# Kernel tuning notes

Hardware: AMD Instinct MI355X
Metric: run time of the kernel (lower is better)

The kernel has to match this reference:

```python
import jax, jax.numpy as jnp
import numpy as np

D_MODEL = 128
NHEAD = 8
HEAD_DIM = D_MODEL // NHEAD  # 16
NUM_LAYERS = 7
NUM_LABELS = 2
N_NODES = 10000
N_EDGES = 160000
NEG_SLOPE = 0.2  # GATv2Conv default negative_slope


def setup_inputs() -> dict:
    key = jax.random.key(0)
    ks = jax.random.split(key, 10)
    s = 1.0 / np.sqrt(D_MODEL)
    inp = {}
    inp["x"] = jax.random.normal(ks[0], (N_NODES, D_MODEL), dtype=jnp.float32)
    inp["edge_index"] = jax.random.randint(ks[1], (2, N_EDGES), 0, N_NODES, dtype=jnp.int64)
    inp["nchunks"] = 8  # uniform extra chunk size -> chunk = NUM_LABELS + 8 = 10
    # per-layer GATv2 params, stacked on a leading layer axis
    inp["Wl"] = jax.random.normal(ks[2], (NUM_LAYERS, D_MODEL, NHEAD * HEAD_DIM), dtype=jnp.float32) * s
    inp["bl"] = jnp.zeros((NUM_LAYERS, NHEAD * HEAD_DIM), dtype=jnp.float32)
    inp["Wr"] = jax.random.normal(ks[3], (NUM_LAYERS, D_MODEL, NHEAD * HEAD_DIM), dtype=jnp.float32) * s
    inp["br"] = jnp.zeros((NUM_LAYERS, NHEAD * HEAD_DIM), dtype=jnp.float32)
    inp["att"] = jax.random.normal(ks[4], (NUM_LAYERS, NHEAD, HEAD_DIM), dtype=jnp.float32) * s
    inp["bias"] = jnp.zeros((NUM_LAYERS, NHEAD * HEAD_DIM), dtype=jnp.float32)
    # split head: Linear(d_model, 1)
    inp["w_head"] = jax.random.normal(ks[5], (D_MODEL, 1), dtype=jnp.float32) * s
    inp["b_head"] = jnp.zeros((1,), dtype=jnp.float32)
    return inp


def _gatv2_layer(x, src, dst, Wl, bl, Wr, br, att, bias):
    # GATv2: e_ij = a^T LeakyReLU(W_l x_j + W_r x_i); alpha = segment-softmax over dst; out_i = sum alpha * W_l x_j
    N = x.shape[0]
    xl = (x @ Wl + bl).reshape(N, NHEAD, HEAD_DIM)
    xr = (x @ Wr + br).reshape(N, NHEAD, HEAD_DIM)
    z = jax.nn.leaky_relu(xl[src] + xr[dst], NEG_SLOPE)          # [E, H, D]
    e = jnp.einsum('ehd,hd->eh', z, att)                          # [E, H]
    emax = jax.ops.segment_max(e, dst, num_segments=N)            # [N, H]
    ex = jnp.exp(e - emax[dst])
    denom = jax.ops.segment_sum(ex, dst, num_segments=N)          # [N, H]
    alpha = ex / (denom[dst] + 1e-16)                             # [E, H]
    out = jax.ops.segment_sum(alpha[..., None] * xl[src], dst, num_segments=N)  # [N, H, D]
    return out.reshape(N, NHEAD * HEAD_DIM) + bias


def reference(x, edge_index, nchunks, Wl, bl, Wr, br, att, bias, w_head, b_head):
    N = x.shape[0]
    loop = jnp.arange(N, dtype=edge_index.dtype)  # GATv2Conv add_self_loops=True
    src = jnp.concatenate([edge_index[0], loop])
    dst = jnp.concatenate([edge_index[1], loop])
    for i in range(NUM_LAYERS):
        x = _gatv2_layer(x, src, dst, Wl[i], bl[i], Wr[i], br[i], att[i], bias[i])
    # uniform split of size (NUM_LABELS + nchunks); keep first NUM_LABELS rows of each chunk
    chunk = NUM_LABELS + int(nchunks)
    xs = x.reshape(-1, chunk, D_MODEL)[:, :NUM_LABELS]            # [n_chunks, num_labels, d]
    out = (xs @ w_head + b_head)[..., 0]                          # [n_chunks, num_labels]
    return out
```

## Files before the change

### kernel.cpp

```cpp
#include <hip/hip_runtime.h>
#include <math.h>

typedef __attribute__((ext_vector_type(8))) short bf16x8;
typedef __attribute__((ext_vector_type(4))) float f32x4;

#define WFRAG (16 * 4 * 64 * 8)


__device__ inline int detect_is64(const int* __restrict__ ei) {
    int is64 = 1;
#pragma unroll
    for (int k = 1; k < 16; k += 2) is64 &= (ei[k] == 0);
    return is64;
}

__device__ inline void split1(float f, short& hi, short& lo) {
    unsigned u = __float_as_uint(f);
    hi = (short)(u >> 16);
    float fl = f - __uint_as_float(u & 0xffff0000u);
    lo = (short)(__float_as_uint(fl) >> 16);
}

__device__ inline void cvt8(const float4& a, const float4& b, bf16x8& hi, bf16x8& lo) {
    float f[8] = {a.x, a.y, a.z, a.w, b.x, b.y, b.z, b.w};
#pragma unroll
    for (int j = 0; j < 8; j++) {
        unsigned u = __float_as_uint(f[j]);
        hi[j] = (short)(u >> 16);
        float fl = f[j] - __uint_as_float(u & 0xffff0000u);
        lo[j] = (short)(__float_as_uint(fl) >> 16);
    }
}


__global__ __launch_bounds__(256) void prologue(const float* __restrict__ Wl,
                                                const float* __restrict__ Wr,
                                                short* __restrict__ Whi,
                                                short* __restrict__ Wlo,
                                                const float4* __restrict__ x4,
                                                short* __restrict__ cvH,
                                                short* __restrict__ cvL,
                                                const int* __restrict__ ei,
                                                int* __restrict__ deg,
                                                int N, int E) {
    __shared__ float Wt[128][17];
    int b = blockIdx.x, t = threadIdx.x;
    if (b < 112) {
        int l = b >> 4;
        int tile = b & 15;
        int c0 = tile * 16;
        const float* Wsrc = (c0 < 128) ? Wl + (size_t)l * 16384 : Wr + (size_t)l * 16384;
        int cbase = (c0 < 128) ? c0 : c0 - 128;
#pragma unroll
        for (int it = 0; it < 8; it++) {
            int idx = it * 256 + t;
            int k = idx >> 4, c = idx & 15;
            Wt[k][c] = Wsrc[(size_t)k * 128 + cbase + c];
        }
        __syncthreads();
        int kt = t >> 6, lane = t & 63, q = (lane >> 4), cl = lane & 15;
        bf16x8 hi, lo;
#pragma unroll
        for (int j = 0; j < 8; j++) {
            short h, lw;
            split1(Wt[kt * 32 + q * 8 + j][cl], h, lw);
            hi[j] = h; lo[j] = lw;
        }
        size_t off = ((((size_t)l * 16 + tile) * 4 + kt) * 64 + lane) * 8;
        *(bf16x8*)(Whi + off) = hi;
        *(bf16x8*)(Wlo + off) = lo;
        return;
    }
    int rb = b - 112;
    int RB = gridDim.x - 112;
    int n8 = N * 16;
    for (int id = rb * 256 + t; id < n8; id += RB * 256) {
        float4 a = x4[2 * id];
        float4 bb = x4[2 * id + 1];
        bf16x8 h, lw;
        cvt8(a, bb, h, lw);
        *(bf16x8*)(cvH + (size_t)id * 8) = h;
        *(bf16x8*)(cvL + (size_t)id * 8) = lw;
    }
    int is64 = detect_is64(ei);
    for (int e = rb * 256 + t; e < E; e += RB * 256) {
        long long pos = (long long)E + e;
        int d = ei[is64 ? 2 * pos : pos];
        if ((unsigned)d < (unsigned)N) atomicAdd(&deg[d], 1);
    }
}


__global__ __launch_bounds__(1024) void scan_kernel(const int* __restrict__ deg,
                                                    int* __restrict__ off,
                                                    int* __restrict__ cur, int N) {
    __shared__ int wsum[16];
    int t = threadIdx.x;
    int per = (N + 1023) >> 10;
    int b0 = t * per;
    int s = 0;
    for (int k = 0; k < per; k++) {
        int idx = b0 + k;
        if (idx < N) s += deg[idx];
    }
    int lane = t & 63, w = t >> 6;
    int v = s;
#pragma unroll
    for (int o = 1; o < 64; o <<= 1) {
        int u = __shfl_up(v, o, 64);
        if (lane >= o) v += u;
    }
    if (lane == 63) wsum[w] = v;
    __syncthreads();
    if (t == 0) {
        int r = 0;
#pragma unroll
        for (int j = 0; j < 16; j++) { int xx = wsum[j]; wsum[j] = r; r += xx; }
        off[N] = r;
    }
    __syncthreads();
    int run = v - s + wsum[w];
    for (int k = 0; k < per; k++) {
        int idx = b0 + k;
        if (idx < N) {
            off[idx] = run;
            cur[idx] = run;
            run += deg[idx];
        }
    }
}

__global__ void fill_kernel(const int* __restrict__ ei, int E, int N,
                            int* __restrict__ cur, int* __restrict__ esrc) {
    int e = blockIdx.x * blockDim.x + threadIdx.x;
    if (e >= E) return;
    int is64 = detect_is64(ei);
    long long spos = e, dpos = (long long)E + e;
    int s = ei[is64 ? 2 * spos : spos];
    int d = ei[is64 ? 2 * dpos : dpos];
    if ((unsigned)d >= (unsigned)N || (unsigned)s >= (unsigned)N) return;
    int p = atomicAdd(&cur[d], 1);
    esrc[p] = s;
}


__global__ __launch_bounds__(512, 1) void gemm_xlxr(const short* __restrict__ xhi,
                                                    const short* __restrict__ xlo,
                                                    const short* __restrict__ WhiL,
                                                    const short* __restrict__ WloL,
                                                    const float* __restrict__ blv,
                                                    const float* __restrict__ brv,
                                                    float* __restrict__ xl,
                                                    float* __restrict__ xr,
                                                    int N, int ntiles) {
    int t = threadIdx.x;
    int w = t >> 6, lane = t & 63, q = lane >> 4, cl = lane & 15;

    bf16x8 Bh[2][4], Bl[2][4];
    float biasv[2];
    float* op[2];
    int colc[2];
#pragma unroll
    for (int nt = 0; nt < 2; nt++) {
        int tile = w * 2 + nt;
        int col = tile * 16 + cl;
        if (col < 128) { biasv[nt] = blv[col]; op[nt] = xl; colc[nt] = col; }
        else           { biasv[nt] = brv[col - 128]; op[nt] = xr; colc[nt] = col - 128; }
#pragma unroll
        for (int kt = 0; kt < 4; kt++) {
            size_t o = (((size_t)tile * 4 + kt) * 64 + lane) * 8;
            Bh[nt][kt] = *(const bf16x8*)(WhiL + o);
            Bl[nt][kt] = *(const bf16x8*)(WloL + o);
        }
    }

    for (int rt = blockIdx.x; rt < ntiles; rt += gridDim.x) {
        int row = rt * 16 + cl;
        if (row >= N) row = N - 1;
        const short* ph = xhi + (size_t)row * 128 + q * 8;
        const short* pl = xlo + (size_t)row * 128 + q * 8;
        bf16x8 AH[4], AL[4];
#pragma unroll
        for (int kt = 0; kt < 4; kt++) {
            AH[kt] = *(const bf16x8*)(ph + kt * 32);
            AL[kt] = *(const bf16x8*)(pl + kt * 32);
        }

        f32x4 acc0 = {0.f, 0.f, 0.f, 0.f}, acc1 = {0.f, 0.f, 0.f, 0.f};
#pragma unroll
        for (int kt = 0; kt < 4; kt++) {
            acc0 = __builtin_amdgcn_mfma_f32_16x16x32_bf16(AH[kt], Bh[0][kt], acc0, 0, 0, 0);
            acc1 = __builtin_amdgcn_mfma_f32_16x16x32_bf16(AH[kt], Bh[1][kt], acc1, 0, 0, 0);
            acc0 = __builtin_amdgcn_mfma_f32_16x16x32_bf16(AL[kt], Bh[0][kt], acc0, 0, 0, 0);
            acc1 = __builtin_amdgcn_mfma_f32_16x16x32_bf16(AL[kt], Bh[1][kt], acc1, 0, 0, 0);
            acc0 = __builtin_amdgcn_mfma_f32_16x16x32_bf16(AH[kt], Bl[0][kt], acc0, 0, 0, 0);
            acc1 = __builtin_amdgcn_mfma_f32_16x16x32_bf16(AH[kt], Bl[1][kt], acc1, 0, 0, 0);
        }

#pragma unroll
        for (int nt = 0; nt < 2; nt++) {
            f32x4 a = nt ? acc1 : acc0;
#pragma unroll
            for (int r = 0; r < 4; r++) {
                int orow = rt * 16 + q * 4 + r;
                if (orow < N) op[nt][(size_t)orow * 128 + colc[nt]] = a[r] + biasv[nt];
            }
        }
    }
}


__device__ inline void agg_node(int i, int sub, int cl,
                                const float4* __restrict__ xl4, const float4* __restrict__ xr4,
                                const int* __restrict__ off, const int* __restrict__ esrc,
                                float4 atA, float4 atB, float4 bA, float4 bB,
                                float4& oA, float4& oB) {
    float4 xrA = xr4[(size_t)i * 32 + 2 * cl];
    float4 xrB = xr4[(size_t)i * 32 + 2 * cl + 1];
    int start = off[i];
    int total = off[i + 1] - start + 1;
    int groups = (total + 3) >> 2;

    int k0 = sub;
    int s0 = (k0 < total) ? ((k0 == 0) ? i : esrc[start + k0 - 1]) : i;
    int k1 = 4 + sub;
    int s1 = (k1 < total) ? esrc[start + k1 - 1] : i;
    float4 v0A = xl4[(size_t)s0 * 32 + 2 * cl];
    float4 v0B = xl4[(size_t)s0 * 32 + 2 * cl + 1];
    int k2 = 8 + sub;
    int s2 = (k2 < total) ? esrc[start + k2 - 1] : i;
    float4 v1A = xl4[(size_t)s1 * 32 + 2 * cl];
    float4 v1B = xl4[(size_t)s1 * 32 + 2 * cl + 1];

    float s = 0.f;
    float4 aA = make_float4(0.f, 0.f, 0.f, 0.f);
    float4 aB = make_float4(0.f, 0.f, 0.f, 0.f);

    for (int g = 0; g < groups; g++) {
        int k3 = 4 * (g + 3) + sub;
        int s3 = (k3 < total) ? esrc[start + k3 - 1] : i;
        float4 v2A = xl4[(size_t)s2 * 32 + 2 * cl];
        float4 v2B = xl4[(size_t)s2 * 32 + 2 * cl + 1];

        int kc = 4 * g + sub;
        int valid = kc < total;
        float z0 = v0A.x + xrA.x, z1 = v0A.y + xrA.y, z2 = v0A.z + xrA.z, z3 = v0A.w + xrA.w;
        float z4 = v0B.x + xrB.x, z5 = v0B.y + xrB.y, z6 = v0B.z + xrB.z, z7 = v0B.w + xrB.w;
        z0 = (z0 > 0.f) ? z0 : 0.2f * z0;
        z1 = (z1 > 0.f) ? z1 : 0.2f * z1;
        z2 = (z2 > 0.f) ? z2 : 0.2f * z2;
        z3 = (z3 > 0.f) ? z3 : 0.2f * z3;
        z4 = (z4 > 0.f) ? z4 : 0.2f * z4;
        z5 = (z5 > 0.f) ? z5 : 0.2f * z5;
        z6 = (z6 > 0.f) ? z6 : 0.2f * z6;
        z7 = (z7 > 0.f) ? z7 : 0.2f * z7;
        float p = z0 * atA.x + z1 * atA.y + z2 * atA.z + z3 * atA.w
                + z4 * atB.x + z5 * atB.y + z6 * atB.z + z7 * atB.w;
        p += __shfl_xor(p, 1, 64);
        p = fminf(fmaxf(p, -80.f), 80.f);
        float wgt = valid ? __expf(p) : 0.f;
        s += wgt;
        aA.x += wgt * v0A.x; aA.y += wgt * v0A.y; aA.z += wgt * v0A.z; aA.w += wgt * v0A.w;
        aB.x += wgt * v0B.x; aB.y += wgt * v0B.y; aB.z += wgt * v0B.z; aB.w += wgt * v0B.w;

        v0A = v1A; v0B = v1B;
        v1A = v2A; v1B = v2B;
        s2 = s3;
    }

#pragma unroll
    for (int o = 16; o <= 32; o <<= 1) {
        s += __shfl_xor(s, o, 64);
        aA.x += __shfl_xor(aA.x, o, 64); aA.y += __shfl_xor(aA.y, o, 64);
        aA.z += __shfl_xor(aA.z, o, 64); aA.w += __shfl_xor(aA.w, o, 64);
        aB.x += __shfl_xor(aB.x, o, 64); aB.y += __shfl_xor(aB.y, o, 64);
        aB.z += __shfl_xor(aB.z, o, 64); aB.w += __shfl_xor(aB.w, o, 64);
    }
    float inv = 1.f / (s + 1e-16f);
    oA.x = aA.x * inv + bA.x; oA.y = aA.y * inv + bA.y;
    oA.z = aA.z * inv + bA.z; oA.w = aA.w * inv + bA.w;
    oB.x = aB.x * inv + bB.x; oB.y = aB.y * inv + bB.y;
    oB.z = aB.z * inv + bB.z; oB.w = aB.w * inv + bB.w;
}


__global__ __launch_bounds__(256) void agg_gemm(const float4* __restrict__ xl4,
                                                const float4* __restrict__ xr4,
                                                const int* __restrict__ off,
                                                const int* __restrict__ esrc,
                                                const float4* __restrict__ att4,
                                                const float4* __restrict__ bias4,
                                                const short* __restrict__ WhiL,
                                                const short* __restrict__ WloL,
                                                const float* __restrict__ blv,
                                                const float* __restrict__ brv,
                                                float* __restrict__ xlo_out,
                                                float* __restrict__ xro_out,
                                                int N) {
    __shared__ __align__(16) short hiL[16 * 136];
    __shared__ __align__(16) short loL[16 * 136];
    int t = threadIdx.x;
    int w = t >> 6, lane = t & 63, sub = lane >> 4, cl = lane & 15, q = lane >> 4;
    int base = blockIdx.x * 16;

    float4 atA = att4[2 * cl];
    float4 atB = att4[2 * cl + 1];
    float4 bA = bias4[2 * cl], bB = bias4[2 * cl + 1];

    for (int j = 0; j < 4; j++) {
        int i = base + w * 4 + j;
        if (i < N) {
            float4 oA, oB;
            agg_node(i, sub, cl, xl4, xr4, off, esrc, atA, atB, bA, bB, oA, oB);
            if (sub == 0) {
                bf16x8 h, lw;
                cvt8(oA, oB, h, lw);
                int r = w * 4 + j;
                *(bf16x8*)&hiL[r * 136 + cl * 8] = h;
                *(bf16x8*)&loL[r * 136 + cl * 8] = lw;
            }
        }
    }
    __syncthreads();

    bf16x8 Ah[4], Al[4];
#pragma unroll
    for (int kt = 0; kt < 4; kt++) {
        Ah[kt] = *(const bf16x8*)&hiL[cl * 136 + kt * 32 + q * 8];
        Al[kt] = *(const bf16x8*)&loL[cl * 136 + kt * 32 + q * 8];
    }

#pragma unroll
    for (int tt = 0; tt < 4; tt++) {
        int tile = w * 4 + tt;
        int col = tile * 16 + cl;
        f32x4 acc = {0.f, 0.f, 0.f, 0.f};
#pragma unroll
        for (int kt = 0; kt < 4; kt++) {
            size_t o = (((size_t)tile * 4 + kt) * 64 + lane) * 8;
            bf16x8 bh = *(const bf16x8*)(WhiL + o);
            bf16x8 bl2 = *(const bf16x8*)(WloL + o);
            acc = __builtin_amdgcn_mfma_f32_16x16x32_bf16(Ah[kt], bh, acc, 0, 0, 0);
            acc = __builtin_amdgcn_mfma_f32_16x16x32_bf16(Al[kt], bh, acc, 0, 0, 0);
            acc = __builtin_amdgcn_mfma_f32_16x16x32_bf16(Ah[kt], bl2, acc, 0, 0, 0);
        }
        float biasv;
        float* op;
        int cc;
        if (col < 128) { biasv = blv[col]; op = xlo_out; cc = col; }
        else           { biasv = brv[col - 128]; op = xro_out; cc = col - 128; }
#pragma unroll
        for (int r = 0; r < 4; r++) {
            int row = base + q * 4 + r;
            if (row < N) op[(size_t)row * 128 + cc] = acc[r] + biasv;
        }
    }
}


__global__ __launch_bounds__(256) void gat_agg(const float4* __restrict__ xl4,
                                               const float4* __restrict__ xr4,
                                               const int* __restrict__ off,
                                               const int* __restrict__ esrc,
                                               const float4* __restrict__ att4,
                                               const float4* __restrict__ bias4,
                                               float4* __restrict__ out4, int N) {
    int lane = threadIdx.x & 63;
    int sub = lane >> 4;
    int cl = lane & 15;
    int i = blockIdx.x * 4 + (threadIdx.x >> 6);
    if (i >= N) return;
    float4 atA = att4[2 * cl];
    float4 atB = att4[2 * cl + 1];
    float4 bA = bias4[2 * cl], bB = bias4[2 * cl + 1];
    float4 oA, oB;
    agg_node(i, sub, cl, xl4, xr4, off, esrc, atA, atB, bA, bB, oA, oB);
    if (sub == 0) {
        out4[(size_t)i * 32 + 2 * cl] = oA;
        out4[(size_t)i * 32 + 2 * cl + 1] = oB;
    }
}


__global__ __launch_bounds__(128) void head_kernel(const float* __restrict__ x,
                                                   const float* __restrict__ w,
                                                   const float* __restrict__ bh,
                                                   const int* __restrict__ nch,
                                                   float* __restrict__ out) {
    __shared__ float r[2];
    int b = blockIdx.x, t = threadIdx.x;
    int chunk = 2 + nch[0];
    int row = (b >> 1) * chunk + (b & 1);
    float p = x[(size_t)row * 128 + t] * w[t];
#pragma unroll
    for (int o = 32; o >= 1; o >>= 1) p += __shfl_xor(p, o, 64);
    if ((t & 63) == 0) r[t >> 6] = p;
    __syncthreads();
    if (t == 0) out[b] = r[0] + r[1] + bh[0];
}


extern "C" void kernel_launch(void* const* d_in, const int* in_sizes, int n_in,
                              void* d_out, int out_size, void* d_ws, size_t ws_size,
                              hipStream_t stream) {
    const float* x0 = (const float*)d_in[0];
    const int* ei = (const int*)d_in[1];
    const int* nchunks = (const int*)d_in[2];
    const float* Wl = (const float*)d_in[3];
    const float* bl = (const float*)d_in[4];
    const float* Wr = (const float*)d_in[5];
    const float* br = (const float*)d_in[6];
    const float* att = (const float*)d_in[7];
    const float* bias = (const float*)d_in[8];
    const float* wh = (const float*)d_in[9];
    const float* bh = (const float*)d_in[10];

    const int D = 128;
    int N = in_sizes[0] / D;
    int E = in_sizes[1] / 2;
    int ntiles = (N + 15) / 16;

    size_t fN = (size_t)N * D;
    float* xlA = (float*)d_ws;
    float* xrA = xlA + fN;
    float* xlB = xrA + fN;
    float* xrB = xlB + fN;
    float* xout = xrB + fN;
    short* cvH0 = (short*)(xout + fN);
    short* cvL0 = cvH0 + fN;
    short* Whi = cvL0 + fN;
    short* Wlo = Whi + 7 * (size_t)WFRAG;
    int* deg = (int*)(Wlo + 7 * (size_t)WFRAG);
    int* off = deg + N;
    int* cur = off + N + 1;
    int* esrc = cur + N;

    hipMemsetAsync(deg, 0, (size_t)N * sizeof(int), stream);
    prologue<<<112 + 640, 256, 0, stream>>>(Wl, Wr, Whi, Wlo, (const float4*)x0,
                                            cvH0, cvL0, ei, deg, N, E);
    scan_kernel<<<1, 1024, 0, stream>>>(deg, off, cur, N);
    fill_kernel<<<(E + 255) / 256, 256, 0, stream>>>(ei, E, N, cur, esrc);

    gemm_xlxr<<<256, 512, 0, stream>>>(cvH0, cvL0, Whi, Wlo, bl, br, xlA, xrA, N, ntiles);

    for (int l = 0; l < 6; l++) {
        const float* rxl = (l % 2 == 0) ? xlA : xlB;
        const float* rxr = (l % 2 == 0) ? xrA : xrB;
        float* wxl = (l % 2 == 0) ? xlB : xlA;
        float* wxr = (l % 2 == 0) ? xrB : xrA;
        agg_gemm<<<ntiles, 256, 0, stream>>>((const float4*)rxl, (const float4*)rxr, off, esrc,
                                             (const float4*)(att + (size_t)l * D),
                                             (const float4*)(bias + (size_t)l * D),
                                             Whi + (size_t)(l + 1) * WFRAG,
                                             Wlo + (size_t)(l + 1) * WFRAG,
                                             bl + (size_t)(l + 1) * D,
                                             br + (size_t)(l + 1) * D,
                                             wxl, wxr, N);
    }

    gat_agg<<<(N + 3) / 4, 256, 0, stream>>>((const float4*)xlA, (const float4*)xrA, off, esrc,
                                             (const float4*)(att + 6 * (size_t)D),
                                             (const float4*)(bias + 6 * (size_t)D),
                                             (float4*)xout, N);

    head_kernel<<<out_size, 128, 0, stream>>>(xout, wh, bh, nchunks, (float*)d_out);
}
```

Measured before the change: 272.8 us.

## Split fused agg+GEMM into head-sliced aggregation and separate GEMM kernels

Replaces the fused per-layer aggregation+MFMA GEMM kernel with two kernels. The first is a head-sliced aggregation: each block handles one head for 16 nodes, with 4 lanes per edge slot, and writes a bf16 hi/lo split. The second is a standalone GEMM with the weights held in registers. The scan is also merged with the first GEMM into one launch. This aims to raise parallelism and locality in the gather phase, at the cost of extra launches and an intermediate buffer round trip each layer.

```diff
diff --git a/kernel.cpp b/kernel.cpp
--- a/kernel.cpp
+++ b/kernel.cpp
@@ -2,6 +2,7 @@
 #include <math.h>
 
 typedef __attribute__((ext_vector_type(8))) short bf16x8;
+typedef __attribute__((ext_vector_type(4))) short short4v;
 typedef __attribute__((ext_vector_type(4))) float f32x4;
 
 #define WFRAG (16 * 4 * 64 * 8)
@@ -91,41 +92,173 @@
 }
 
 
-__global__ __launch_bounds__(1024) void scan_kernel(const int* __restrict__ deg,
-                                                    int* __restrict__ off,
-                                                    int* __restrict__ cur, int N) {
-    __shared__ int wsum[16];
+__global__ __launch_bounds__(512, 1) void scan_gemm0(const int* __restrict__ deg,
+                                                     int* __restrict__ offp,
+                                                     int* __restrict__ cur, int N,
+                                                     const short* __restrict__ xhi,
+                                                     const short* __restrict__ xlo,
+                                                     const short* __restrict__ WhiL,
+                                                     const short* __restrict__ WloL,
+                                                     const float* __restrict__ blv,
+                                                     const float* __restrict__ brv,
+                                                     float* __restrict__ xl,
+                                                     float* __restrict__ xr,
+                                                     int ntiles) {
+    __shared__ int wsum[8];
     int t = threadIdx.x;
-    int per = (N + 1023) >> 10;
-    int b0 = t * per;
-    int s = 0;
-    for (int k = 0; k < per; k++) {
-        int idx = b0 + k;
-        if (idx < N) s += deg[idx];
-    }
-    int lane = t & 63, w = t >> 6;
-    int v = s;
-#pragma unroll
-    for (int o = 1; o < 64; o <<= 1) {
-        int u = __shfl_up(v, o, 64);
-        if (lane >= o) v += u;
-    }
-    if (lane == 63) wsum[w] = v;
-    __syncthreads();
-    if (t == 0) {
-        int r = 0;
-#pragma unroll
-        for (int j = 0; j < 16; j++) { int xx = wsum[j]; wsum[j] = r; r += xx; }
-        off[N] = r;
-    }
-    __syncthreads();
-    int run = v - s + wsum[w];
-    for (int k = 0; k < per; k++) {
-        int idx = b0 + k;
-        if (idx < N) {
-            off[idx] = run;
-            cur[idx] = run;
-            run += deg[idx];
+    if (blockIdx.x == 0) {
+        int per = (N + 511) >> 9;
+        int b0 = t * per;
+        int s = 0;
+        for (int k = 0; k < per; k++) {
+            int idx = b0 + k;
+            if (idx < N) s += deg[idx];
+        }
+        int lane = t & 63, w = t >> 6;
+        int v = s;
+#pragma unroll
+        for (int o = 1; o < 64; o <<= 1) {
+            int u = __shfl_up(v, o, 64);
+            if (lane >= o) v += u;
+        }
+        if (lane == 63) wsum[w] = v;
+        __syncthreads();
+        if (t == 0) {
+            int r = 0;
+#pragma unroll
+            for (int j = 0; j < 8; j++) { int xx = wsum[j]; wsum[j] = r; r += xx; }
+            offp[N] = r;
+        }
+        __syncthreads();
+        int run = v - s + wsum[w];
+        for (int k = 0; k < per; k++) {
+            int idx = b0 + k;
+            if (idx < N) {
+                offp[idx] = run;
+                cur[idx] = run;
+                run += deg[idx];
+            }
+        }
+        return;
+    }
+
+    int w = t >> 6, lane = t & 63, q = lane >> 4, cl = lane & 15;
+
+    bf16x8 Bh[2][4], Bl[2][4];
+    float biasv[2];
+    float* op[2];
+    int colc[2];
+#pragma unroll
+    for (int nt = 0; nt < 2; nt++) {
+        int tile = w * 2 + nt;
+        int col = tile * 16 + cl;
+        if (col < 128) { biasv[nt] = blv[col]; op[nt] = xl; colc[nt] = col; }
+        else           { biasv[nt] = brv[col - 128]; op[nt] = xr; colc[nt] = col - 128; }
+#pragma unroll
+        for (int kt = 0; kt < 4; kt++) {
+            size_t o = (((size_t)tile * 4 + kt) * 64 + lane) * 8;
+            Bh[nt][kt] = *(const bf16x8*)(WhiL + o);
+            Bl[nt][kt] = *(const bf16x8*)(WloL + o);
+        }
+    }
+
+    for (int rt = blockIdx.x - 1; rt < ntiles; rt += gridDim.x - 1) {
+        int row = rt * 16 + cl;
+        if (row >= N) row = N - 1;
+        const short* ph = xhi + (size_t)row * 128 + q * 8;
+        const short* pl = xlo + (size_t)row * 128 + q * 8;
+        bf16x8 AH[4], AL[4];
+#pragma unroll
+        for (int kt = 0; kt < 4; kt++) {
+            AH[kt] = *(const bf16x8*)(ph + kt * 32);
+            AL[kt] = *(const bf16x8*)(pl + kt * 32);
+        }
+
+        f32x4 acc0 = {0.f, 0.f, 0.f, 0.f}, acc1 = {0.f, 0.f, 0.f, 0.f};
+#pragma unroll
+        for (int kt = 0; kt < 4; kt++) {
+            acc0 = __builtin_amdgcn_mfma_f32_16x16x32_bf16(AH[kt], Bh[0][kt], acc0, 0, 0, 0);
+            acc1 = __builtin_amdgcn_mfma_f32_16x16x32_bf16(AH[kt], Bh[1][kt], acc1, 0, 0, 0);
+            acc0 = __builtin_amdgcn_mfma_f32_16x16x32_bf16(AL[kt], Bh[0][kt], acc0, 0, 0, 0);
+            acc1 = __builtin_amdgcn_mfma_f32_16x16x32_bf16(AL[kt], Bh[1][kt], acc1, 0, 0, 0);
+            acc0 = __builtin_amdgcn_mfma_f32_16x16x32_bf16(AH[kt], Bl[0][kt], acc0, 0, 0, 0);
+            acc1 = __builtin_amdgcn_mfma_f32_16x16x32_bf16(AH[kt], Bl[1][kt], acc1, 0, 0, 0);
+        }
+
+#pragma unroll
+        for (int nt = 0; nt < 2; nt++) {
+            f32x4 a = nt ? acc1 : acc0;
+#pragma unroll
+            for (int r = 0; r < 4; r++) {
+                int orow = rt * 16 + q * 4 + r;
+                if (orow < N) op[nt][(size_t)orow * 128 + colc[nt]] = a[r] + biasv[nt];
+            }
+        }
+    }
+}
+
+
+__global__ __launch_bounds__(512, 1) void gemm_x(const short* __restrict__ xhi,
+                                                 const short* __restrict__ xlo,
+                                                 const short* __restrict__ WhiL,
+                                                 const short* __restrict__ WloL,
+                                                 const float* __restrict__ blv,
+                                                 const float* __restrict__ brv,
+                                                 float* __restrict__ xl,
+                                                 float* __restrict__ xr,
+                                                 int N, int ntiles) {
+    int t = threadIdx.x;
+    int w = t >> 6, lane = t & 63, q = lane >> 4, cl = lane & 15;
+
+    bf16x8 Bh[2][4], Bl[2][4];
+    float biasv[2];
+    float* op[2];
+    int colc[2];
+#pragma unroll
+    for (int nt = 0; nt < 2; nt++) {
+        int tile = w * 2 + nt;
+        int col = tile * 16 + cl;
+        if (col < 128) { biasv[nt] = blv[col]; op[nt] = xl; colc[nt] = col; }
+        else           { biasv[nt] = brv[col - 128]; op[nt] = xr; colc[nt] = col - 128; }
+#pragma unroll
+        for (int kt = 0; kt < 4; kt++) {
+            size_t o = (((size_t)tile * 4 + kt) * 64 + lane) * 8;
+            Bh[nt][kt] = *(const bf16x8*)(WhiL + o);
+            Bl[nt][kt] = *(const bf16x8*)(WloL + o);
+        }
+    }
+
+    for (int rt = blockIdx.x; rt < ntiles; rt += gridDim.x) {
+        int row = rt * 16 + cl;
+        if (row >= N) row = N - 1;
+        const short* ph = xhi + (size_t)row * 128 + q * 8;
+        const short* pl = xlo + (size_t)row * 128 + q * 8;
+        bf16x8 AH[4], AL[4];
+#pragma unroll
+        for (int kt = 0; kt < 4; kt++) {
+            AH[kt] = *(const bf16x8*)(ph + kt * 32);
+            AL[kt] = *(const bf16x8*)(pl + kt * 32);
+        }
+
+        f32x4 acc0 = {0.f, 0.f, 0.f, 0.f}, acc1 = {0.f, 0.f, 0.f, 0.f};
+#pragma unroll
+        for (int kt = 0; kt < 4; kt++) {
+            acc0 = __builtin_amdgcn_mfma_f32_16x16x32_bf16(AH[kt], Bh[0][kt], acc0, 0, 0, 0);
+            acc1 = __builtin_amdgcn_mfma_f32_16x16x32_bf16(AH[kt], Bh[1][kt], acc1, 0, 0, 0);
+            acc0 = __builtin_amdgcn_mfma_f32_16x16x32_bf16(AL[kt], Bh[0][kt], acc0, 0, 0, 0);
+            acc1 = __builtin_amdgcn_mfma_f32_16x16x32_bf16(AL[kt], Bh[1][kt], acc1, 0, 0, 0);
+            acc0 = __builtin_amdgcn_mfma_f32_16x16x32_bf16(AH[kt], Bl[0][kt], acc0, 0, 0, 0);
+            acc1 = __builtin_amdgcn_mfma_f32_16x16x32_bf16(AH[kt], Bl[1][kt], acc1, 0, 0, 0);
+        }
+
+#pragma unroll
+        for (int nt = 0; nt < 2; nt++) {
+            f32x4 a = nt ? acc1 : acc0;
+#pragma unroll
+            for (int r = 0; r < 4; r++) {
+                int orow = rt * 16 + q * 4 + r;
+                if (orow < N) op[nt][(size_t)orow * 128 + colc[nt]] = a[r] + biasv[nt];
+            }
         }
     }
 }
@@ -144,240 +277,87 @@
 }
 
 
-__global__ __launch_bounds__(512, 1) void gemm_xlxr(const short* __restrict__ xhi,
-                                                    const short* __restrict__ xlo,
-                                                    const short* __restrict__ WhiL,
-                                                    const short* __restrict__ WloL,
-                                                    const float* __restrict__ blv,
-                                                    const float* __restrict__ brv,
-                                                    float* __restrict__ xl,
-                                                    float* __restrict__ xr,
-                                                    int N, int ntiles) {
+__global__ __launch_bounds__(256, 4) void agg_sliced(const float4* __restrict__ xl4,
+                                                     const float4* __restrict__ xr4,
+                                                     const int* __restrict__ off,
+                                                     const int* __restrict__ esrc,
+                                                     const float4* __restrict__ att4,
+                                                     const float4* __restrict__ bias4,
+                                                     short* __restrict__ nhi,
+                                                     short* __restrict__ nlo,
+                                                     float4* __restrict__ out4,
+                                                     int N) {
     int t = threadIdx.x;
-    int w = t >> 6, lane = t & 63, q = lane >> 4, cl = lane & 15;
-
-    bf16x8 Bh[2][4], Bl[2][4];
-    float biasv[2];
-    float* op[2];
-    int colc[2];
-#pragma unroll
-    for (int nt = 0; nt < 2; nt++) {
-        int tile = w * 2 + nt;
-        int col = tile * 16 + cl;
-        if (col < 128) { biasv[nt] = blv[col]; op[nt] = xl; colc[nt] = col; }
-        else           { biasv[nt] = brv[col - 128]; op[nt] = xr; colc[nt] = col - 128; }
-#pragma unroll
-        for (int kt = 0; kt < 4; kt++) {
-            size_t o = (((size_t)tile * 4 + kt) * 64 + lane) * 8;
-            Bh[nt][kt] = *(const bf16x8*)(WhiL + o);
-            Bl[nt][kt] = *(const bf16x8*)(WloL + o);
-        }
-    }
-
-    for (int rt = blockIdx.x; rt < ntiles; rt += gridDim.x) {
-        int row = rt * 16 + cl;
-        if (row >= N) row = N - 1;
-        const short* ph = xhi + (size_t)row * 128 + q * 8;
-        const short* pl = xlo + (size_t)row * 128 + q * 8;
-        bf16x8 AH[4], AL[4];
-#pragma unroll
-        for (int kt = 0; kt < 4; kt++) {
-            AH[kt] = *(const bf16x8*)(ph + kt * 32);
-            AL[kt] = *(const bf16x8*)(pl + kt * 32);
-        }
-
-        f32x4 acc0 = {0.f, 0.f, 0.f, 0.f}, acc1 = {0.f, 0.f, 0.f, 0.f};
-#pragma unroll
-        for (int kt = 0; kt < 4; kt++) {
-            acc0 = __builtin_amdgcn_mfma_f32_16x16x32_bf16(AH[kt], Bh[0][kt], acc0, 0, 0, 0);
-            acc1 = __builtin_amdgcn_mfma_f32_16x16x32_bf16(AH[kt], Bh[1][kt], acc1, 0, 0, 0);
-            acc0 = __builtin_amdgcn_mfma_f32_16x16x32_bf16(AL[kt], Bh[0][kt], acc0, 0, 0, 0);
-            acc1 = __builtin_amdgcn_mfma_f32_16x16x32_bf16(AL[kt], Bh[1][kt], acc1, 0, 0, 0);
-            acc0 = __builtin_amdgcn_mfma_f32_16x16x32_bf16(AH[kt], Bl[0][kt], acc0, 0, 0, 0);
-            acc1 = __builtin_amdgcn_mfma_f32_16x16x32_bf16(AH[kt], Bl[1][kt], acc1, 0, 0, 0);
-        }
-
-#pragma unroll
-        for (int nt = 0; nt < 2; nt++) {
-            f32x4 a = nt ? acc1 : acc0;
-#pragma unroll
-            for (int r = 0; r < 4; r++) {
-                int orow = rt * 16 + q * 4 + r;
-                if (orow < N) op[nt][(size_t)orow * 128 + colc[nt]] = a[r] + biasv[nt];
-            }
-        }
-    }
-}
-
-
-__device__ inline void agg_node(int i, int sub, int cl,
-                                const float4* __restrict__ xl4, const float4* __restrict__ xr4,
-                                const int* __restrict__ off, const int* __restrict__ esrc,
-                                float4 atA, float4 atB, float4 bA, float4 bB,
-                                float4& oA, float4& oB) {
-    float4 xrA = xr4[(size_t)i * 32 + 2 * cl];
-    float4 xrB = xr4[(size_t)i * 32 + 2 * cl + 1];
+    int grp = t >> 4;
+    int u = t & 15, s = u >> 2, fl = u & 3;
+    int h = blockIdx.x & 7;
+    int i = (blockIdx.x >> 3) * 16 + grp;
+    if (i >= N) return;
+    int fidx = h * 4 + fl;
+
+    float4 xr = xr4[(size_t)i * 32 + fidx];
+    float4 at = att4[fidx];
+
     int start = off[i];
     int total = off[i + 1] - start + 1;
     int groups = (total + 3) >> 2;
 
-    int k0 = sub;
+    int k0 = s;
     int s0 = (k0 < total) ? ((k0 == 0) ? i : esrc[start + k0 - 1]) : i;
-    int k1 = 4 + sub;
+    float4 a = xl4[(size_t)s0 * 32 + fidx];
+    int k1 = 4 + s;
     int s1 = (k1 < total) ? esrc[start + k1 - 1] : i;
-    float4 v0A = xl4[(size_t)s0 * 32 + 2 * cl];
-    float4 v0B = xl4[(size_t)s0 * 32 + 2 * cl + 1];
-    int k2 = 8 + sub;
+    float4 b = xl4[(size_t)s1 * 32 + fidx];
+    int k2 = 8 + s;
     int s2 = (k2 < total) ? esrc[start + k2 - 1] : i;
-    float4 v1A = xl4[(size_t)s1 * 32 + 2 * cl];
-    float4 v1B = xl4[(size_t)s1 * 32 + 2 * cl + 1];
-
-    float s = 0.f;
-    float4 aA = make_float4(0.f, 0.f, 0.f, 0.f);
-    float4 aB = make_float4(0.f, 0.f, 0.f, 0.f);
+
+    float denom = 0.f;
+    float4 ac = make_float4(0.f, 0.f, 0.f, 0.f);
 
     for (int g = 0; g < groups; g++) {
-        int k3 = 4 * (g + 3) + sub;
+        float4 c = xl4[(size_t)s2 * 32 + fidx];
+        int k3 = (g + 3) * 4 + s;
         int s3 = (k3 < total) ? esrc[start + k3 - 1] : i;
-        float4 v2A = xl4[(size_t)s2 * 32 + 2 * cl];
-        float4 v2B = xl4[(size_t)s2 * 32 + 2 * cl + 1];
-
-        int kc = 4 * g + sub;
-        int valid = kc < total;
-        float z0 = v0A.x + xrA.x, z1 = v0A.y + xrA.y, z2 = v0A.z + xrA.z, z3 = v0A.w + xrA.w;
-        float z4 = v0B.x + xrB.x, z5 = v0B.y + xrB.y, z6 = v0B.z + xrB.z, z7 = v0B.w + xrB.w;
-        z0 = (z0 > 0.f) ? z0 : 0.2f * z0;
-        z1 = (z1 > 0.f) ? z1 : 0.2f * z1;
-        z2 = (z2 > 0.f) ? z2 : 0.2f * z2;
-        z3 = (z3 > 0.f) ? z3 : 0.2f * z3;
-        z4 = (z4 > 0.f) ? z4 : 0.2f * z4;
-        z5 = (z5 > 0.f) ? z5 : 0.2f * z5;
-        z6 = (z6 > 0.f) ? z6 : 0.2f * z6;
-        z7 = (z7 > 0.f) ? z7 : 0.2f * z7;
-        float p = z0 * atA.x + z1 * atA.y + z2 * atA.z + z3 * atA.w
-                + z4 * atB.x + z5 * atB.y + z6 * atB.z + z7 * atB.w;
+
+        int valid = (g * 4 + s) < total;
+        float z0 = a.x + xr.x; z0 = (z0 > 0.f) ? z0 : 0.2f * z0;
+        float z1 = a.y + xr.y; z1 = (z1 > 0.f) ? z1 : 0.2f * z1;
+        float z2 = a.z + xr.z; z2 = (z2 > 0.f) ? z2 : 0.2f * z2;
+        float z3 = a.w + xr.w; z3 = (z3 > 0.f) ? z3 : 0.2f * z3;
+        float p = z0 * at.x + z1 * at.y + z2 * at.z + z3 * at.w;
         p += __shfl_xor(p, 1, 64);
+        p += __shfl_xor(p, 2, 64);
         p = fminf(fmaxf(p, -80.f), 80.f);
         float wgt = valid ? __expf(p) : 0.f;
-        s += wgt;
-        aA.x += wgt * v0A.x; aA.y += wgt * v0A.y; aA.z += wgt * v0A.z; aA.w += wgt * v0A.w;
-        aB.x += wgt * v0B.x; aB.y += wgt * v0B.y; aB.z += wgt * v0B.z; aB.w += wgt * v0B.w;
-
-        v0A = v1A; v0B = v1B;
-        v1A = v2A; v1B = v2B;
-        s2 = s3;
-    }
-
-#pragma unroll
-    for (int o = 16; o <= 32; o <<= 1) {
-        s += __shfl_xor(s, o, 64);
-        aA.x += __shfl_xor(aA.x, o, 64); aA.y += __shfl_xor(aA.y, o, 64);
-        aA.z += __shfl_xor(aA.z, o, 64); aA.w += __shfl_xor(aA.w, o, 64);
-        aB.x += __shfl_xor(aB.x, o, 64); aB.y += __shfl_xor(aB.y, o, 64);
-        aB.z += __shfl_xor(aB.z, o, 64); aB.w += __shfl_xor(aB.w, o, 64);
-    }
-    float inv = 1.f / (s + 1e-16f);
-    oA.x = aA.x * inv + bA.x; oA.y = aA.y * inv + bA.y;
-    oA.z = aA.z * inv + bA.z; oA.w = aA.w * inv + bA.w;
-    oB.x = aB.x * inv + bB.x; oB.y = aB.y * inv + bB.y;
-    oB.z = aB.z * inv + bB.z; oB.w = aB.w * inv + bB.w;
-}
-
-
-__global__ __launch_bounds__(256) void agg_gemm(const float4* __restrict__ xl4,
-                                                const float4* __restrict__ xr4,
-                                                const int* __restrict__ off,
-                                                const int* __restrict__ esrc,
-                                                const float4* __restrict__ att4,
-                                                const float4* __restrict__ bias4,
-                                                const short* __restrict__ WhiL,
-                                                const short* __restrict__ WloL,
-                                                const float* __restrict__ blv,
-                                                const float* __restrict__ brv,
-                                                float* __restrict__ xlo_out,
-                                                float* __restrict__ xro_out,
-                                                int N) {
-    __shared__ __align__(16) short hiL[16 * 136];
-    __shared__ __align__(16) short loL[16 * 136];
-    int t = threadIdx.x;
-    int w = t >> 6, lane = t & 63, sub = lane >> 4, cl = lane & 15, q = lane >> 4;
-    int base = blockIdx.x * 16;
-
-    float4 atA = att4[2 * cl];
-    float4 atB = att4[2 * cl + 1];
-    float4 bA = bias4[2 * cl], bB = bias4[2 * cl + 1];
-
-    for (int j = 0; j < 4; j++) {
-        int i = base + w * 4 + j;
-        if (i < N) {
-            float4 oA, oB;
-            agg_node(i, sub, cl, xl4, xr4, off, esrc, atA, atB, bA, bB, oA, oB);
-            if (sub == 0) {
-                bf16x8 h, lw;
-                cvt8(oA, oB, h, lw);
-                int r = w * 4 + j;
-                *(bf16x8*)&hiL[r * 136 + cl * 8] = h;
-                *(bf16x8*)&loL[r * 136 + cl * 8] = lw;
-            }
-        }
-    }
-    __syncthreads();
-
-    bf16x8 Ah[4], Al[4];
-#pragma unroll
-    for (int kt = 0; kt < 4; kt++) {
-        Ah[kt] = *(const bf16x8*)&hiL[cl * 136 + kt * 32 + q * 8];
-        Al[kt] = *(const bf16x8*)&loL[cl * 136 + kt * 32 + q * 8];
-    }
-
-#pragma unroll
-    for (int tt = 0; tt < 4; tt++) {
-        int tile = w * 4 + tt;
-        int col = tile * 16 + cl;
-        f32x4 acc = {0.f, 0.f, 0.f, 0.f};
-#pragma unroll
-        for (int kt = 0; kt < 4; kt++) {
-            size_t o = (((size_t)tile * 4 + kt) * 64 + lane) * 8;
-            bf16x8 bh = *(const bf16x8*)(WhiL + o);
-            bf16x8 bl2 = *(const bf16x8*)(WloL + o);
-            acc = __builtin_amdgcn_mfma_f32_16x16x32_bf16(Ah[kt], bh, acc, 0, 0, 0);
-            acc = __builtin_amdgcn_mfma_f32_16x16x32_bf16(Al[kt], bh, acc, 0, 0, 0);
-            acc = __builtin_amdgcn_mfma_f32_16x16x32_bf16(Ah[kt], bl2, acc, 0, 0, 0);
-        }
-        float biasv;
-        float* op;
-        int cc;
-        if (col < 128) { biasv = blv[col]; op = xlo_out; cc = col; }
-        else           { biasv = brv[col - 128]; op = xro_out; cc = col - 128; }
-#pragma unroll
-        for (int r = 0; r < 4; r++) {
-            int row = base + q * 4 + r;
-            if (row < N) op[(size_t)row * 128 + cc] = acc[r] + biasv;
-        }
-    }
-}
-
-
-__global__ __launch_bounds__(256) void gat_agg(const float4* __restrict__ xl4,
-                                               const float4* __restrict__ xr4,
-                                               const int* __restrict__ off,
-                                               const int* __restrict__ esrc,
-                                               const float4* __restrict__ att4,
-                                               const float4* __restrict__ bias4,
-                                               float4* __restrict__ out4, int N) {
-    int lane = threadIdx.x & 63;
-    int sub = lane >> 4;
-    int cl = lane & 15;
-    int i = blockIdx.x * 4 + (threadIdx.x >> 6);
-    if (i >= N) return;
-    float4 atA = att4[2 * cl];
-    float4 atB = att4[2 * cl + 1];
-    float4 bA = bias4[2 * cl], bB = bias4[2 * cl + 1];
-    float4 oA, oB;
-    agg_node(i, sub, cl, xl4, xr4, off, esrc, atA, atB, bA, bB, oA, oB);
-    if (sub == 0) {
-        out4[(size_t)i * 32 + 2 * cl] = oA;
-        out4[(size_t)i * 32 + 2 * cl + 1] = oB;
+        denom += wgt;
+        ac.x += wgt * a.x; ac.y += wgt * a.y; ac.z += wgt * a.z; ac.w += wgt * a.w;
+
+        a = b; b = c; s2 = s3;
+    }
+
+#pragma unroll
+    for (int o = 4; o <= 8; o <<= 1) {
+        denom += __shfl_xor(denom, o, 64);
+        ac.x += __shfl_xor(ac.x, o, 64); ac.y += __shfl_xor(ac.y, o, 64);
+        ac.z += __shfl_xor(ac.z, o, 64); ac.w += __shfl_xor(ac.w, o, 64);
+    }
+    if (s == 0) {
+        float inv = 1.f / (denom + 1e-16f);
+        float4 bi = bias4[fidx];
+        float4 o;
+        o.x = ac.x * inv + bi.x; o.y = ac.y * inv + bi.y;
+        o.z = ac.z * inv + bi.z; o.w = ac.w * inv + bi.w;
+        if (out4) out4[(size_t)i * 32 + fidx] = o;
+        if (nhi) {
+            short4v hv, lv;
+            short hh, ll;
+            split1(o.x, hh, ll); hv[0] = hh; lv[0] = ll;
+            split1(o.y, hh, ll); hv[1] = hh; lv[1] = ll;
+            split1(o.z, hh, ll); hv[2] = hh; lv[2] = ll;
+            split1(o.w, hh, ll); hv[3] = hh; lv[3] = ll;
+            *(short4v*)&nhi[(size_t)i * 128 + h * 16 + fl * 4] = hv;
+            *(short4v*)&nlo[(size_t)i * 128 + h * 16 + fl * 4] = lv;
+        }
     }
 }
 
@@ -421,14 +401,14 @@
     int ntiles = (N + 15) / 16;
 
     size_t fN = (size_t)N * D;
-    float* xlA = (float*)d_ws;
-    float* xrA = xlA + fN;
-    float* xlB = xrA + fN;
-    float* xrB = xlB + fN;
-    float* xout = xrB + fN;
+    float* xl = (float*)d_ws;
+    float* xr = xl + fN;
+    float* xout = xr + fN;
     short* cvH0 = (short*)(xout + fN);
     short* cvL0 = cvH0 + fN;
-    short* Whi = cvL0 + fN;
+    short* cvH1 = cvL0 + fN;
+    short* cvL1 = cvH1 + fN;
+    short* Whi = cvL1 + fN;
     short* Wlo = Whi + 7 * (size_t)WFRAG;
     int* deg = (int*)(Wlo + 7 * (size_t)WFRAG);
     int* off = deg + N;
@@ -438,30 +418,31 @@
     hipMemsetAsync(deg, 0, (size_t)N * sizeof(int), stream);
     prologue<<<112 + 640, 256, 0, stream>>>(Wl, Wr, Whi, Wlo, (const float4*)x0,
                                             cvH0, cvL0, ei, deg, N, E);
-    scan_kernel<<<1, 1024, 0, stream>>>(deg, off, cur, N);
+    scan_gemm0<<<257, 512, 0, stream>>>(deg, off, cur, N, cvH0, cvL0, Whi, Wlo,
+                                        bl, br, xl, xr, ntiles);
     fill_kernel<<<(E + 255) / 256, 256, 0, stream>>>(ei, E, N, cur, esrc);
 
-    gemm_xlxr<<<256, 512, 0, stream>>>(cvH0, cvL0, Whi, Wlo, bl, br, xlA, xrA, N, ntiles);
-
+    int aggblocks = ((N + 15) / 16) * 8;
     for (int l = 0; l < 6; l++) {
-        const float* rxl = (l % 2 == 0) ? xlA : xlB;
-        const float* rxr = (l % 2 == 0) ? xrA : xrB;
-        float* wxl = (l % 2 == 0) ? xlB : xlA;
-        float* wxr = (l % 2 == 0) ? xrB : xrA;
-        agg_gemm<<<ntiles, 256, 0, stream>>>((const float4*)rxl, (const float4*)rxr, off, esrc,
-                                             (const float4*)(att + (size_t)l * D),
-                                             (const float4*)(bias + (size_t)l * D),
-                                             Whi + (size_t)(l + 1) * WFRAG,
-                                             Wlo + (size_t)(l + 1) * WFRAG,
-                                             bl + (size_t)(l + 1) * D,
-                                             br + (size_t)(l + 1) * D,
-                                             wxl, wxr, N);
-    }
-
-    gat_agg<<<(N + 3) / 4, 256, 0, stream>>>((const float4*)xlA, (const float4*)xrA, off, esrc,
-                                             (const float4*)(att + 6 * (size_t)D),
-                                             (const float4*)(bias + 6 * (size_t)D),
-                                             (float4*)xout, N);
+        agg_sliced<<<aggblocks, 256, 0, stream>>>((const float4*)xl, (const float4*)xr,
+                                                  off, esrc,
+                                                  (const float4*)(att + (size_t)l * D),
+                                                  (const float4*)(bias + (size_t)l * D),
+                                                  cvH1, cvL1, (float4*)nullptr, N);
+        gemm_x<<<256, 512, 0, stream>>>(cvH1, cvL1,
+                                        Whi + (size_t)(l + 1) * WFRAG,
+                                        Wlo + (size_t)(l + 1) * WFRAG,
+                                        bl + (size_t)(l + 1) * D,
+                                        br + (size_t)(l + 1) * D,
+                                        xl, xr, N, ntiles);
+    }
+
+    agg_sliced<<<aggblocks, 256, 0, stream>>>((const float4*)xl, (const float4*)xr,
+                                              off, esrc,
+                                              (const float4*)(att + 6 * (size_t)D),
+                                              (const float4*)(bias + 6 * (size_t)D),
+                                              (short*)nullptr, (short*)nullptr,
+                                              (float4*)xout, N);
 
     head_kernel<<<out_size, 128, 0, stream>>>(xout, wh, bh, nchunks, (float*)d_out);
 }
```

After: 316.4 us. 1.16x slower.
